# Kernel optimization log

Measured on AMD Instinct MI355X. Metric: run time of the kernel, lower is better.

The kernel has to match this reference:

```python
import jax, jax.numpy as jnp
import numpy as np

PATCH = 256
CH = 28


def setup_inputs() -> dict:
    key = jax.random.key(0)
    kx, km = jax.random.split(key)
    x = jax.random.normal(kx, (32, PATCH, PATCH, CH), dtype=jnp.float32)
    # bk: binary mask from a (P/2, P/2) random pattern, tiled 2x2, repeated over channels
    ms = PATCH // 2
    bk_fixed = jnp.round(jax.random.uniform(km, (ms, ms), dtype=jnp.float32))
    bk_tile = jnp.tile(bk_fixed, (2, 2))                      # [P, P]
    bk = jnp.repeat(bk_tile[:, :, None], CH, axis=2)          # [P, P, C]
    return {"x": x, "bk": bk}


def reference(x, bk):
    # Original math per channel ch:
    #   y[i,j,ch] = x[(i+ch)%P, j, ch] * bk[i,j,ch]      (roll by -ch, multiply)
    #   z[i,j,ch] = y[(i-ch)%P, j, ch]                   (roll back by +ch)
    # => z[i,j,ch] = x[i,j,ch] * bk[(i-ch)%P, j, ch]
    # So fuse the two rolls into a single per-channel roll of the mask,
    # then a fused multiply + channel-sum (single memory pass).
    C = x.shape[-1]
    shifts = jnp.arange(C)
    # roll each channel of the mask by +ch along height
    bk_shifted = jax.vmap(lambda m, s: jnp.roll(m, s, axis=0),
                          in_axes=(2, 0), out_axes=2)(bk, shifts)  # [P, P, C]
    # fused shift-multiply-accumulate: [B, P, P]
    return jnp.sum(x * bk_shifted[None], axis=-1)
```

## Files before the change

kernel.cpp:

```cpp
#include <hip/hip_runtime.h>

#define P 256
#define C 28
#define NPIX (P * P)
#define MASK_ELEMS (NPIX * C)
#define Q 7
#define BLK 448
#define PIX_PER_BLK 64
#define BLKS_PER_IMG 1024

__global__ __launch_bounds__(256) void prep_mask_kernel(
    const float* __restrict__ bk, float* __restrict__ bks) {
    int idx = blockIdx.x * 256 + threadIdx.x;
    if (idx >= MASK_ELEMS) return;
    int ch = idx % C;
    int ij = idx / C;
    int j = ij & (P - 1);
    int i = ij >> 8;
    int src_row = (i - ch) & (P - 1);
    bks[idx] = bk[(src_row * P + j) * C + ch];
}

__global__ __launch_bounds__(BLK) void codednet_f4_kernel(
    const float4* __restrict__ x4, const float4* __restrict__ m4,
    float* __restrict__ out) {
    __shared__ float s[BLK];
    int t = threadIdx.x;
    int f = blockIdx.x * BLK + t;
    int mf = (blockIdx.x & (BLKS_PER_IMG - 1)) * BLK + t;
    float4 a = x4[f];
    float4 m = m4[mf];
    s[t] = a.x * m.x + a.y * m.y + a.z * m.z + a.w * m.w;
    __syncthreads();
    if (t < PIX_PER_BLK) {
        const float* p = s + t * Q;
        float acc = ((p[0] + p[1]) + (p[2] + p[3])) + ((p[4] + p[5]) + p[6]);
        out[blockIdx.x * PIX_PER_BLK + t] = acc;
    }
}

__global__ __launch_bounds__(256) void codednet_inline_kernel(
    const float* __restrict__ x, const float* __restrict__ bk,
    float* __restrict__ out) {
    int pid = blockIdx.x * 256 + threadIdx.x;
    int pix = pid & (NPIX - 1);
    int j = pix & (P - 1);
    int i = pix >> 8;
    const float* xp = x + (size_t)pid * C;
    float acc = 0.f;
#pragma unroll
    for (int ch = 0; ch < C; ++ch) {
        int src_row = (i - ch) & (P - 1);
        acc += xp[ch] * bk[(src_row * P + j) * C + ch];
    }
    out[pid] = acc;
}

extern "C" void kernel_launch(void* const* d_in, const int* in_sizes, int n_in,
                              void* d_out, int out_size, void* d_ws, size_t ws_size,
                              hipStream_t stream) {
    const float* x  = (const float*)d_in[0];
    const float* bk = (const float*)d_in[1];
    float* out = (float*)d_out;

    const int total = out_size;

    if (ws_size >= (size_t)MASK_ELEMS * sizeof(float)) {
        float* bks = (float*)d_ws;
        prep_mask_kernel<<<(MASK_ELEMS + 255) / 256, 256, 0, stream>>>(bk, bks);
        const int nblocks = total / PIX_PER_BLK;
        codednet_f4_kernel<<<nblocks, BLK, 0, stream>>>(
            (const float4*)x, (const float4*)bks, out);
    } else {
        codednet_inline_kernel<<<(total + 255) / 256, 256, 0, stream>>>(x, bk, out);
    }
}
```

Measured before the change: 321.5 us.

## Fuse mask shift into main kernel and reuse mask across batch loop

Removes the separate mask-precompute kernel and its workspace round trip. Each block now gathers its shifted mask values once and loops over all 32 images with a one-step register prefetch of the next image's x. The mask is read once instead of per image, but the grid shrinks from 32768 to 1024 blocks. Each iteration also adds two barriers, which may cut occupancy and memory-level parallelism.

```diff
diff --git a/kernel.cpp b/kernel.cpp
--- a/kernel.cpp
+++ b/kernel.cpp
@@ -3,57 +3,47 @@
 #define P 256
 #define C 28
 #define NPIX (P * P)
-#define MASK_ELEMS (NPIX * C)
+#define NB 32
 #define Q 7
 #define BLK 448
 #define PIX_PER_BLK 64
-#define BLKS_PER_IMG 1024
+#define F4_PER_IMG (NPIX * Q)
 
-__global__ __launch_bounds__(256) void prep_mask_kernel(
-    const float* __restrict__ bk, float* __restrict__ bks) {
-    int idx = blockIdx.x * 256 + threadIdx.x;
-    if (idx >= MASK_ELEMS) return;
-    int ch = idx % C;
-    int ij = idx / C;
-    int j = ij & (P - 1);
-    int i = ij >> 8;
-    int src_row = (i - ch) & (P - 1);
-    bks[idx] = bk[(src_row * P + j) * C + ch];
-}
-
-__global__ __launch_bounds__(BLK) void codednet_f4_kernel(
-    const float4* __restrict__ x4, const float4* __restrict__ m4,
+__global__ __launch_bounds__(BLK) void codednet_fused_kernel(
+    const float4* __restrict__ x4, const float* __restrict__ bk,
     float* __restrict__ out) {
     __shared__ float s[BLK];
-    int t = threadIdx.x;
-    int f = blockIdx.x * BLK + t;
-    int mf = (blockIdx.x & (BLKS_PER_IMG - 1)) * BLK + t;
-    float4 a = x4[f];
-    float4 m = m4[mf];
-    s[t] = a.x * m.x + a.y * m.y + a.z * m.z + a.w * m.w;
-    __syncthreads();
-    if (t < PIX_PER_BLK) {
-        const float* p = s + t * Q;
-        float acc = ((p[0] + p[1]) + (p[2] + p[3])) + ((p[4] + p[5]) + p[6]);
-        out[blockIdx.x * PIX_PER_BLK + t] = acc;
+    const int t = threadIdx.x;
+    const int p = t / Q;
+    const int k = t - p * Q;
+    const int pixbase = blockIdx.x * PIX_PER_BLK;
+    const int pixel = pixbase + p;
+    const int i = pixel >> 8;
+    const int j = pixel & (P - 1);
+    const int ch0 = 4 * k;
+
+    const float4* xp = x4 + (size_t)blockIdx.x * BLK + t;
+    float4 a = xp[0];
+
+    float4 m;
+    m.x = bk[(((i - (ch0 + 0)) & (P - 1)) * P + j) * C + (ch0 + 0)];
+    m.y = bk[(((i - (ch0 + 1)) & (P - 1)) * P + j) * C + (ch0 + 1)];
+    m.z = bk[(((i - (ch0 + 2)) & (P - 1)) * P + j) * C + (ch0 + 2)];
+    m.w = bk[(((i - (ch0 + 3)) & (P - 1)) * P + j) * C + (ch0 + 3)];
+
+    for (int b = 0; b < NB; ++b) {
+        float4 nxt = a;
+        if (b + 1 < NB) nxt = xp[(size_t)(b + 1) * F4_PER_IMG];
+        s[t] = a.x * m.x + a.y * m.y + a.z * m.z + a.w * m.w;
+        __syncthreads();
+        if (t < PIX_PER_BLK) {
+            const float* q = s + t * Q;
+            out[(size_t)b * NPIX + pixbase + t] =
+                ((q[0] + q[1]) + (q[2] + q[3])) + ((q[4] + q[5]) + q[6]);
+        }
+        __syncthreads();
+        a = nxt;
     }
-}
-
-__global__ __launch_bounds__(256) void codednet_inline_kernel(
-    const float* __restrict__ x, const float* __restrict__ bk,
-    float* __restrict__ out) {
-    int pid = blockIdx.x * 256 + threadIdx.x;
-    int pix = pid & (NPIX - 1);
-    int j = pix & (P - 1);
-    int i = pix >> 8;
-    const float* xp = x + (size_t)pid * C;
-    float acc = 0.f;
-#pragma unroll
-    for (int ch = 0; ch < C; ++ch) {
-        int src_row = (i - ch) & (P - 1);
-        acc += xp[ch] * bk[(src_row * P + j) * C + ch];
-    }
-    out[pid] = acc;
 }
 
 extern "C" void kernel_launch(void* const* d_in, const int* in_sizes, int n_in,
@@ -62,16 +52,8 @@
     const float* x  = (const float*)d_in[0];
     const float* bk = (const float*)d_in[1];
     float* out = (float*)d_out;
+    (void)d_ws; (void)ws_size; (void)in_sizes; (void)n_in; (void)out_size;
 
-    const int total = out_size;
-
-    if (ws_size >= (size_t)MASK_ELEMS * sizeof(float)) {
-        float* bks = (float*)d_ws;
-        prep_mask_kernel<<<(MASK_ELEMS + 255) / 256, 256, 0, stream>>>(bk, bks);
-        const int nblocks = total / PIX_PER_BLK;
-        codednet_f4_kernel<<<nblocks, BLK, 0, stream>>>(
-            (const float4*)x, (const float4*)bks, out);
-    } else {
-        codednet_inline_kernel<<<(total + 255) / 256, 256, 0, stream>>>(x, bk, out);
-    }
+    codednet_fused_kernel<<<NPIX / PIX_PER_BLK, BLK, 0, stream>>>(
+        (const float4*)x, bk, out);
 }
```

Measured after the change: 324.5 us. About the same (+0.9%).
